# Performance work log

Measured on AMD Instinct MI355X. Metric: run time of the kernel, lower is better.

The kernel has to match this reference:

```python
import jax, jax.numpy as jnp
import numpy as np

PI = 3.1415927410125732
N = 4096
VELOCITY = 5e-7
RC = 3.15e-6          # collision radius
RR = 8e-6             # repulsion radius
RO = 2.5e-5           # orientation radius (Ra = inf -> inside_Ra all-true)
ALPHA = PI            # field of view; < 2*pi so within_view masking is active
DT_TRANS = 1.4e-14    # translational diffusion DT
DR = 0.0028
GAMMA = 25.0
DT = 0.2              # timestep dt
COLLISION_ITERS = 3   # fixed-iteration version of recursive solve_collisions
EPS = 1e-14


def _c(x):  # [N,2] real -> complex64
    return jax.lax.complex(x[..., 0], x[..., 1])


def _r(z):  # complex -> [..., 2] real
    return jnp.stack([z.real, z.imag], axis=-1)


def _anglediff(a, b):
    # torch get_anglediff: wrap angle(a)-angle(b) into (-pi, pi)
    diff = jnp.angle(a) - jnp.angle(b)
    diff = jnp.where(diff <= -PI, jnp.mod(diff, PI), diff)
    return diff - (diff >= PI) * (2.0 * PI)


def _cossim(a, b):
    # nn.CosineSimilarity(dim=1, eps=1e-14) on view_as_real of complex vectors
    dot = a.real * b.real + a.imag * b.imag
    na = jnp.sqrt(a.real ** 2 + a.imag ** 2 + 1e-30)
    nb = jnp.sqrt(b.real ** 2 + b.imag ** 2 + 1e-30)
    return dot / (jnp.maximum(na, EPS) * jnp.maximum(nb, EPS))


def setup_inputs() -> dict:
    key = jax.random.key(0)
    k1, k2, k3, k4, k5 = jax.random.split(key, 5)
    positions = jax.random.normal(k1, (N, 2), jnp.float32) * 5e-4
    ang = jax.random.uniform(k2, (N,), jnp.float32, -PI, PI)
    orientations = jnp.stack([jnp.cos(ang), jnp.sin(ang)], axis=-1)  # unit complex
    Deltas = jax.random.uniform(k3, (1,), jnp.float32, 0.1, 0.6)
    rot_noise = jax.random.normal(k4, (N,), jnp.float32)
    trans_noise = jax.random.normal(k5, (N, 2), jnp.float32)
    return {"positions": positions, "orientations": orientations, "Deltas": Deltas,
            "rot_noise": rot_noise, "trans_noise": trans_noise}


def reference(positions, orientations, Deltas, rot_noise, trans_noise):
    p = _c(positions)      # [N] complex positions
    u = _c(orientations)   # [N] complex orientations
    n = p.shape[0]
    eye = jnp.eye(n, dtype=bool)

    # pairwise direction/distance: dirs[i,j] = p_j - p_i
    dirs = p[None, :] - p[:, None]
    dists = jnp.abs(dirs)

    inside_Rr = (dists <= RR) & ~eye
    inside_Ro = dists <= RO + RC
    # inside_Ra with Ra = inf is all-True

    # angle between separation vector and orientation of the *neighbor* j
    ang_diff = _anglediff(dirs, u[None, :])
    in_front = ang_diff < PI / 2
    within_view = ang_diff < ALPHA  # alpha < 2*pi branch active

    cdtype = p.dtype
    mask_rr = (inside_Rr & in_front).astype(cdtype)
    mask_ra = within_view.astype(cdtype)  # inside_Ra all True
    mask_ro = (inside_Ro & within_view).astype(cdtype)

    n_r = mask_rr.real.sum(axis=1)
    S = (mask_rr @ p) / jnp.maximum(n_r, 1.0) - p * jnp.sign(n_r)
    d = -S

    n_a = mask_ra.real.sum(axis=1)
    cms = (mask_ra @ p) / jnp.maximum(n_a, 1.0)
    Ps = cms - p * jnp.sign(n_a)

    orientation_sums = mask_ro @ u

    leftturns = Ps * jnp.exp(1j * Deltas)
    rightturns = Ps * jnp.exp(-1j * Deltas)

    # T >= T_release branch: pick the turn most aligned with neighbor orientations
    left_closer = _cossim(leftturns, orientation_sums) >= _cossim(rightturns, orientation_sums)
    best_turns = jnp.where(left_closer, leftturns, rightturns)

    d_abs = jnp.abs(d)
    d_safe = jnp.where(d_abs > 0, d, jnp.ones((), cdtype))
    best_safe = jnp.where(jnp.abs(best_turns) > 0, best_turns, jnp.ones((), cdtype))
    angle_to_target = jnp.where(d_abs > 0, _anglediff(d_safe, u), _anglediff(best_safe, u))

    # rotational_noise = randn * sqrt(2*DR); rotation = exp(i*(dt*Gamma*DR*sin + noise*sqrt(dt)))
    rot = jnp.exp(1j * (DT * GAMMA * DR * jnp.sin(angle_to_target)
                        + rot_noise * np.float32(np.sqrt(2 * DR)) * np.float32(np.sqrt(DT))))

    # complex-normal translational noise (per-component std 1/sqrt(2)) * sqrt(2*DT) * sqrt(dt)
    tn = _c(trans_noise) * np.float32(np.sqrt(0.5)) * np.float32(np.sqrt(2 * DT_TRANS))
    translation = DT * VELOCITY * u + tn * np.float32(np.sqrt(DT))

    def collide(i, pos):
        dd = pos[None, :] - pos[:, None]
        dd_nd = jnp.where(eye, jnp.ones((), pos.dtype), dd)  # avoid 0/0 on diagonal
        ab = jnp.where(eye, 0.0, jnp.abs(dd_nd))
        coll = ab <= 2 * RC - jnp.eye(n, dtype=ab.dtype)
        safe = jnp.where(coll, ab, 1.0)
        move = jnp.where(coll, dd / safe * ((2.1 * RC - ab) * 0.5), jnp.zeros((), pos.dtype))
        return pos - move.sum(axis=1)

    new_p = jax.lax.fori_loop(0, COLLISION_ITERS, collide, p + translation)
    new_u = u * rot

    # pack the 5 complex outputs as real [5, N, 2]
    return jnp.stack([_r(new_p), _r(new_u), _r(orientation_sums), _r(leftturns), _r(rightturns)], axis=0)
```

## Files before the change

kernel.cpp:

```cpp
#include <hip/hip_runtime.h>
#include <math.h>

#define NPART 4096
#define NBLK  512
#define NTHR  256
#define IPB   8
#define SMAX  256
#define PPT   (NPART / NTHR)

constexpr float RORC   = (float)(2.5e-5 + 3.15e-6);
constexpr float RORC2  = RORC * RORC;
constexpr float RRF    = 8e-6f;
constexpr float RR2    = RRF * RRF;
constexpr float TWORC  = (float)(2.0 * 3.15e-6);
constexpr float TWORC2 = TWORC * TWORC;
constexpr float C21RC  = (float)(2.1 * 3.15e-6);
constexpr float RCAND2 = 1.6e-9f;
constexpr float C_ROT  = (float)(0.2 * 25.0 * 0.0028);
constexpr float C_RN1  = (float)0.07483314773547883;
constexpr float C_SQDT = (float)0.4472135954999579;
constexpr float C_TRV  = (float)(0.2 * 5e-7);
constexpr float C_HALF = (float)0.7071067811865476;
constexpr float C_SQ2T = (float)1.6733200530681511e-07;
constexpr float EPSF   = 1e-14f;

__global__ __launch_bounds__(NTHR, 2) void fused_all(
        const float2* __restrict__ pos, const float2* __restrict__ ori,
        const float* __restrict__ Deltas, const float* __restrict__ rot_noise,
        const float2* __restrict__ trans_noise, float2* __restrict__ out) {
    __shared__ float4   posL4[NPART / 2];
    __shared__ float4   oriL4[NPART / 2];
    __shared__ float    sred[2 * NTHR];
    __shared__ float    res[5][IPB];
    __shared__ unsigned bmap[NPART / 32];
    __shared__ int      Sidx[SMAX];
    __shared__ float4   posS4[SMAX / 2];
    __shared__ int      scnt;
    float2* posL = (float2*)posL4;
    float2* oriL = (float2*)oriL4;
    float2* posS = (float2*)posS4;

    const int tid  = threadIdx.x;
    const int il   = tid >> 6;
    const int lane = tid & 63;
    const int ia   = blockIdx.x * IPB + il;
    const int ib   = ia + 4;

    if (tid == 0) scnt = IPB;
    if (tid < IPB) Sidx[tid] = blockIdx.x * IPB + tid;
    if (tid < NPART / 32) bmap[tid] = 0u;

    float mx = 0.f, my = 0.f;
    #pragma unroll
    for (int k = 0; k < PPT; ++k) {
        const float2 v = pos[k * NTHR + tid];
        const float2 u = ori[k * NTHR + tid];
        posL[k * NTHR + tid] = v;
        oriL[k * NTHR + tid] = u;
        mx += v.x; my += v.y;
    }
    sred[tid] = mx; sred[NTHR + tid] = my;
    __syncthreads();

    const float2 pa = posL[ia];
    const float2 pb = posL[ib];
    float nrA = 0.f, sxA = 0.f, syA = 0.f, oxA = 0.f, oyA = 0.f;
    float nrB = 0.f, sxB = 0.f, syB = 0.f, oxB = 0.f, oyB = 0.f;
    #pragma unroll 2
    for (int t = lane; t < NPART / 2; t += 64) {
        const float4 w = posL4[t];
        const float dxa0 = w.x - pa.x, dya0 = w.y - pa.y;
        const float dxb0 = w.x - pb.x, dyb0 = w.y - pb.y;
        const float dxa1 = w.z - pa.x, dya1 = w.w - pa.y;
        const float dxb1 = w.z - pb.x, dyb1 = w.w - pb.y;
        const float r2a0 = fmaf(dxa0, dxa0, dya0 * dya0);
        const float r2b0 = fmaf(dxb0, dxb0, dyb0 * dyb0);
        const float r2a1 = fmaf(dxa1, dxa1, dya1 * dya1);
        const float r2b1 = fmaf(dxb1, dxb1, dyb1 * dyb1);

        if (r2a0 <= RCAND2 || r2b0 <= RCAND2) {
            const int j = 2 * t;
            atomicOr(&bmap[j >> 5], 1u << (j & 31));
        }
        if (r2a0 <= RORC2 || r2b0 <= RORC2) {
            const float2 uj = oriL[2 * t];
            if (r2a0 <= RORC2) {
                oxA += uj.x; oyA += uj.y;
                if (r2a0 <= RR2 && r2a0 > 0.f) {
                    const float dt_ = fmaf(dxa0, uj.x, dya0 * uj.y);
                    const float cr_ = fmaf(dya0, uj.x, -dxa0 * uj.y);
                    if (!((dt_ <= 0.f) && (cr_ >= 0.f))) {
                        nrA += 1.f; sxA += w.x; syA += w.y;
                    }
                }
            }
            if (r2b0 <= RORC2) {
                oxB += uj.x; oyB += uj.y;
                if (r2b0 <= RR2 && r2b0 > 0.f) {
                    const float dt_ = fmaf(dxb0, uj.x, dyb0 * uj.y);
                    const float cr_ = fmaf(dyb0, uj.x, -dxb0 * uj.y);
                    if (!((dt_ <= 0.f) && (cr_ >= 0.f))) {
                        nrB += 1.f; sxB += w.x; syB += w.y;
                    }
                }
            }
        }
        if (r2a1 <= RCAND2 || r2b1 <= RCAND2) {
            const int j = 2 * t + 1;
            atomicOr(&bmap[j >> 5], 1u << (j & 31));
        }
        if (r2a1 <= RORC2 || r2b1 <= RORC2) {
            const float2 uj = oriL[2 * t + 1];
            if (r2a1 <= RORC2) {
                oxA += uj.x; oyA += uj.y;
                if (r2a1 <= RR2 && r2a1 > 0.f) {
                    const float dt_ = fmaf(dxa1, uj.x, dya1 * uj.y);
                    const float cr_ = fmaf(dya1, uj.x, -dxa1 * uj.y);
                    if (!((dt_ <= 0.f) && (cr_ >= 0.f))) {
                        nrA += 1.f; sxA += w.z; syA += w.w;
                    }
                }
            }
            if (r2b1 <= RORC2) {
                oxB += uj.x; oyB += uj.y;
                if (r2b1 <= RR2 && r2b1 > 0.f) {
                    const float dt_ = fmaf(dxb1, uj.x, dyb1 * uj.y);
                    const float cr_ = fmaf(dyb1, uj.x, -dxb1 * uj.y);
                    if (!((dt_ <= 0.f) && (cr_ >= 0.f))) {
                        nrB += 1.f; sxB += w.z; syB += w.w;
                    }
                }
            }
        }
    }
    {
        float vals[10] = {nrA, sxA, syA, oxA, oyA, nrB, sxB, syB, oxB, oyB};
        #pragma unroll
        for (int q = 0; q < 10; ++q)
            #pragma unroll
            for (int off = 32; off >= 1; off >>= 1)
                vals[q] += __shfl_down(vals[q], off);
        if (lane == 0) {
            res[0][il]     = vals[0]; res[1][il]     = vals[1];
            res[2][il]     = vals[2]; res[3][il]     = vals[3];
            res[4][il]     = vals[4];
            res[0][il + 4] = vals[5]; res[1][il + 4] = vals[6];
            res[2][il + 4] = vals[7]; res[3][il + 4] = vals[8];
            res[4][il + 4] = vals[9];
        }
    }
    __syncthreads();

    if (tid < NPART / 32) {
        unsigned bits = bmap[tid];
        if (tid == (int)(blockIdx.x >> 2))
            bits &= ~(0xFFu << ((blockIdx.x & 3) * 8));
        while (bits) {
            const int b = __ffs(bits) - 1;
            bits &= bits - 1;
            const int slot = atomicAdd(&scnt, 1);
            if (slot < SMAX) Sidx[slot] = tid * 32 + b;
        }
    }
    __syncthreads();
    const int nS = (scnt < SMAX) ? scnt : SMAX;

    if (tid < nS) {
        const int p = Sidx[tid];
        const float2 pq = posL[p];
        const float2 uu = oriL[p];
        const float2 tn = trans_noise[p];
        posS[tid] = make_float2(
            pq.x + (C_TRV * uu.x + ((tn.x * C_HALF) * C_SQ2T) * C_SQDT),
            pq.y + (C_TRV * uu.y + ((tn.y * C_HALF) * C_SQ2T) * C_SQDT));
    }

    for (int s = NTHR / 2; s > 0; s >>= 1) {
        if (tid < s) { sred[tid] += sred[tid + s]; sred[NTHR + tid] += sred[NTHR + tid + s]; }
        __syncthreads();
    }
    const float cmx = sred[0]    * (1.f / NPART);
    const float cmy = sred[NTHR] * (1.f / NPART);

    if (tid < IPB) {
        const int g2 = blockIdx.x * IPB + tid;
        const float2 p = posL[g2];
        const float2 u = oriL[g2];
        const float nrv = res[0][tid], sxv = res[1][tid], syv = res[2][tid];
        const float osx = res[3][tid], osy = res[4][tid];

        const float inv = 1.f / fmaxf(nrv, 1.f);
        const float sg  = (nrv > 0.f) ? 1.f : 0.f;
        const float Sx = sxv * inv - p.x * sg;
        const float Sy = syv * inv - p.y * sg;
        const float dxv = -Sx, dyv = -Sy;

        const float Psx = cmx - p.x;
        const float Psy = cmy - p.y;

        float sd, cd;
        sincosf(Deltas[0], &sd, &cd);
        const float Lx = Psx * cd - Psy * sd;
        const float Ly = Psx * sd + Psy * cd;
        const float Rx = Psx * cd + Psy * sd;
        const float Ry = Psy * cd - Psx * sd;

        const float no  = fmaxf(sqrtf(osx * osx + osy * osy + 1e-30f), EPSF);
        const float nl  = fmaxf(sqrtf(Lx * Lx + Ly * Ly + 1e-30f), EPSF);
        const float nrr = fmaxf(sqrtf(Rx * Rx + Ry * Ry + 1e-30f), EPSF);
        const float csl = (Lx * osx + Ly * osy) / (nl * no);
        const float csr = (Rx * osx + Ry * osy) / (nrr * no);
        const bool left = (csl >= csr);
        const float bx = left ? Lx : Rx;
        const float by = left ? Ly : Ry;

        float cx, cy;
        if (dxv != 0.f || dyv != 0.f)    { cx = dxv; cy = dyv; }
        else if (bx != 0.f || by != 0.f) { cx = bx;  cy = by;  }
        else                             { cx = 1.f; cy = 0.f; }

        const float dt_ = cx * u.x + cy * u.y;
        const float cr_ = cy * u.x - cx * u.y;
        const float sin_t = cr_ / sqrtf(dt_ * dt_ + cr_ * cr_);

        const float ang = C_ROT * sin_t + (rot_noise[g2] * C_RN1) * C_SQDT;
        float sa, ca;
        sincosf(ang, &sa, &ca);
        out[1 * NPART + g2] = make_float2(u.x * ca - u.y * sa,
                                          u.x * sa + u.y * ca);
        out[2 * NPART + g2] = make_float2(osx, osy);
        out[3 * NPART + g2] = make_float2(Lx, Ly);
        out[4 * NPART + g2] = make_float2(Rx, Ry);
    }
    __syncthreads();

    for (int pass = 0; pass < 3; ++pass) {
        float px = 0.f, py = 0.f, ax = 0.f, ay = 0.f;
        const bool mv = (tid < nS);
        if (mv) { px = posS[tid].x; py = posS[tid].y; }
        int b = 0;
        for (; b + 4 <= nS; b += 4) {
            const float4 w0 = posS4[(b >> 1)];
            const float4 w1 = posS4[(b >> 1) + 1];
            const float bxs[4] = {w0.x, w0.z, w1.x, w1.z};
            const float bys[4] = {w0.y, w0.w, w1.y, w1.w};
            #pragma unroll
            for (int s = 0; s < 4; ++s) {
                if (mv) {
                    const float dx = bxs[s] - px, dy = bys[s] - py;
                    const float r2 = fmaf(dx, dx, dy * dy);
                    if (r2 <= TWORC2 && r2 > 0.f) {
                        const float ab = sqrtf(r2);
                        const float sc = (C21RC - ab) * 0.5f / ab;
                        ax = fmaf(dx, sc, ax);
                        ay = fmaf(dy, sc, ay);
                    }
                }
            }
        }
        for (; b < nS; ++b) {
            const float2 pb2 = posS[b];
            if (mv) {
                const float dx = pb2.x - px, dy = pb2.y - py;
                const float r2 = fmaf(dx, dx, dy * dy);
                if (r2 <= TWORC2 && r2 > 0.f) {
                    const float ab = sqrtf(r2);
                    const float sc = (C21RC - ab) * 0.5f / ab;
                    ax = fmaf(dx, sc, ax);
                    ay = fmaf(dy, sc, ay);
                }
            }
        }
        __syncthreads();
        if (mv) posS[tid] = make_float2(px - ax, py - ay);
        __syncthreads();
    }
    if (tid < IPB)
        out[0 * NPART + blockIdx.x * IPB + tid] = posS[tid];
}

extern "C" void kernel_launch(void* const* d_in, const int* in_sizes, int n_in,
                              void* d_out, int out_size, void* d_ws, size_t ws_size,
                              hipStream_t stream) {
    const float2* pos = (const float2*)d_in[0];
    const float2* ori = (const float2*)d_in[1];
    const float*  del = (const float*)d_in[2];
    const float*  rn  = (const float*)d_in[3];
    const float2* tn  = (const float2*)d_in[4];
    float2* o2 = (float2*)d_out;
    (void)d_ws; (void)ws_size;

    fused_all<<<dim3(NBLK), dim3(NTHR), 0, stream>>>(pos, ori, del, rn, tn, o2);
}
```

Measured before the change: 92.10 us.

## Stream pair positions from global memory instead of staging into LDS

Removes the 64KB LDS staging of positions and orientations, so the pair loop reads positions from global/L2 with explicit register double-buffering and fetches orientations on demand. The cut in LDS use lets launch_bounds rise to 4 blocks per CU for more occupancy. The center-of-mass reduction moves after the pair loop, becomes a partial tree plus a wavefront shuffle with fewer barriers, and one barrier before the collision passes is dropped. Scattered global reads of ori and more L2 traffic per block are the tradeoff.

```diff
diff --git a/kernel.cpp b/kernel.cpp
--- a/kernel.cpp
+++ b/kernel.cpp
@@ -24,21 +24,18 @@
 constexpr float C_SQ2T = (float)1.6733200530681511e-07;
 constexpr float EPSF   = 1e-14f;
 
-__global__ __launch_bounds__(NTHR, 2) void fused_all(
+__global__ __launch_bounds__(NTHR, 4) void fused_all(
         const float2* __restrict__ pos, const float2* __restrict__ ori,
         const float* __restrict__ Deltas, const float* __restrict__ rot_noise,
         const float2* __restrict__ trans_noise, float2* __restrict__ out) {
-    __shared__ float4   posL4[NPART / 2];
-    __shared__ float4   oriL4[NPART / 2];
     __shared__ float    sred[2 * NTHR];
     __shared__ float    res[5][IPB];
     __shared__ unsigned bmap[NPART / 32];
     __shared__ int      Sidx[SMAX];
     __shared__ float4   posS4[SMAX / 2];
     __shared__ int      scnt;
-    float2* posL = (float2*)posL4;
-    float2* oriL = (float2*)oriL4;
     float2* posS = (float2*)posS4;
+    const float4* __restrict__ pos4 = (const float4*)pos;
 
     const int tid  = threadIdx.x;
     const int il   = tid >> 6;
@@ -46,29 +43,20 @@
     const int ia   = blockIdx.x * IPB + il;
     const int ib   = ia + 4;
 
+    const float2 pa   = pos[ia];
+    const float2 pb   = pos[ib];
+    const float  delv = Deltas[0];
+    float rn_early = 0.f;
+    if (tid < IPB) rn_early = rot_noise[blockIdx.x * IPB + tid];
+
     if (tid == 0) scnt = IPB;
     if (tid < IPB) Sidx[tid] = blockIdx.x * IPB + tid;
     if (tid < NPART / 32) bmap[tid] = 0u;
-
-    float mx = 0.f, my = 0.f;
-    #pragma unroll
-    for (int k = 0; k < PPT; ++k) {
-        const float2 v = pos[k * NTHR + tid];
-        const float2 u = ori[k * NTHR + tid];
-        posL[k * NTHR + tid] = v;
-        oriL[k * NTHR + tid] = u;
-        mx += v.x; my += v.y;
-    }
-    sred[tid] = mx; sred[NTHR + tid] = my;
     __syncthreads();
 
-    const float2 pa = posL[ia];
-    const float2 pb = posL[ib];
     float nrA = 0.f, sxA = 0.f, syA = 0.f, oxA = 0.f, oyA = 0.f;
     float nrB = 0.f, sxB = 0.f, syB = 0.f, oxB = 0.f, oyB = 0.f;
-    #pragma unroll 2
-    for (int t = lane; t < NPART / 2; t += 64) {
-        const float4 w = posL4[t];
+    auto pair2 = [&](const float4& w, int jbase) {
         const float dxa0 = w.x - pa.x, dya0 = w.y - pa.y;
         const float dxb0 = w.x - pb.x, dyb0 = w.y - pb.y;
         const float dxa1 = w.z - pa.x, dya1 = w.w - pa.y;
@@ -79,11 +67,10 @@
         const float r2b1 = fmaf(dxb1, dxb1, dyb1 * dyb1);
 
         if (r2a0 <= RCAND2 || r2b0 <= RCAND2) {
-            const int j = 2 * t;
-            atomicOr(&bmap[j >> 5], 1u << (j & 31));
+            atomicOr(&bmap[jbase >> 5], 1u << (jbase & 31));
         }
         if (r2a0 <= RORC2 || r2b0 <= RORC2) {
-            const float2 uj = oriL[2 * t];
+            const float2 uj = ori[jbase];
             if (r2a0 <= RORC2) {
                 oxA += uj.x; oyA += uj.y;
                 if (r2a0 <= RR2 && r2a0 > 0.f) {
@@ -106,11 +93,11 @@
             }
         }
         if (r2a1 <= RCAND2 || r2b1 <= RCAND2) {
-            const int j = 2 * t + 1;
-            atomicOr(&bmap[j >> 5], 1u << (j & 31));
+            const int j1 = jbase + 1;
+            atomicOr(&bmap[j1 >> 5], 1u << (j1 & 31));
         }
         if (r2a1 <= RORC2 || r2b1 <= RORC2) {
-            const float2 uj = oriL[2 * t + 1];
+            const float2 uj = ori[jbase + 1];
             if (r2a1 <= RORC2) {
                 oxA += uj.x; oyA += uj.y;
                 if (r2a1 <= RR2 && r2a1 > 0.f) {
@@ -131,6 +118,24 @@
                     }
                 }
             }
+        }
+    };
+    {
+        float4 wb0 = pos4[lane],       wb1 = pos4[lane + 64];
+        float4 wb2 = pos4[lane + 128], wb3 = pos4[lane + 192];
+        #pragma unroll
+        for (int bi = 0; bi < 8; ++bi) {
+            const int t0 = lane + bi * 256;
+            float4 wn0, wn1, wn2, wn3;
+            if (bi < 7) {
+                wn0 = pos4[t0 + 256]; wn1 = pos4[t0 + 320];
+                wn2 = pos4[t0 + 384]; wn3 = pos4[t0 + 448];
+            }
+            pair2(wb0, 2 * t0);
+            pair2(wb1, 2 * (t0 + 64));
+            pair2(wb2, 2 * (t0 + 128));
+            pair2(wb3, 2 * (t0 + 192));
+            if (bi < 7) { wb0 = wn0; wb1 = wn1; wb2 = wn2; wb3 = wn3; }
         }
     }
     {
@@ -149,9 +154,19 @@
             res[4][il + 4] = vals[9];
         }
     }
+
+    float mx = 0.f, my = 0.f;
+    #pragma unroll
+    for (int k = 0; k < PPT; ++k) {
+        const float2 v = pos[k * NTHR + tid];
+        mx += v.x; my += v.y;
+    }
+    sred[tid] = mx; sred[NTHR + tid] = my;
     __syncthreads();
 
-    if (tid < NPART / 32) {
+    if (tid < 128) {
+        sred[tid]        += sred[tid + 128];
+        sred[NTHR + tid] += sred[NTHR + tid + 128];
         unsigned bits = bmap[tid];
         if (tid == (int)(blockIdx.x >> 2))
             bits &= ~(0xFFu << ((blockIdx.x & 3) * 8));
@@ -165,27 +180,38 @@
     __syncthreads();
     const int nS = (scnt < SMAX) ? scnt : SMAX;
 
+    if (tid < 64) {
+        sred[tid]        += sred[tid + 64];
+        sred[NTHR + tid] += sred[NTHR + tid + 64];
+    }
     if (tid < nS) {
         const int p = Sidx[tid];
-        const float2 pq = posL[p];
-        const float2 uu = oriL[p];
+        const float2 pq = pos[p];
+        const float2 uu = ori[p];
         const float2 tn = trans_noise[p];
         posS[tid] = make_float2(
             pq.x + (C_TRV * uu.x + ((tn.x * C_HALF) * C_SQ2T) * C_SQDT),
             pq.y + (C_TRV * uu.y + ((tn.y * C_HALF) * C_SQ2T) * C_SQDT));
     }
-
-    for (int s = NTHR / 2; s > 0; s >>= 1) {
-        if (tid < s) { sred[tid] += sred[tid + s]; sred[NTHR + tid] += sred[NTHR + tid + s]; }
-        __syncthreads();
-    }
-    const float cmx = sred[0]    * (1.f / NPART);
-    const float cmy = sred[NTHR] * (1.f / NPART);
+    __syncthreads();
+
+    float cmx = 0.f, cmy = 0.f;
+    if (il == 0) {
+        float vx = sred[lane];
+        float vy = sred[NTHR + lane];
+        #pragma unroll
+        for (int off = 32; off >= 1; off >>= 1) {
+            vx += __shfl_down(vx, off);
+            vy += __shfl_down(vy, off);
+        }
+        cmx = __shfl(vx, 0) * (1.f / NPART);
+        cmy = __shfl(vy, 0) * (1.f / NPART);
+    }
 
     if (tid < IPB) {
         const int g2 = blockIdx.x * IPB + tid;
-        const float2 p = posL[g2];
-        const float2 u = oriL[g2];
+        const float2 p = pos[g2];
+        const float2 u = ori[g2];
         const float nrv = res[0][tid], sxv = res[1][tid], syv = res[2][tid];
         const float osx = res[3][tid], osy = res[4][tid];
 
@@ -199,7 +225,7 @@
         const float Psy = cmy - p.y;
 
         float sd, cd;
-        sincosf(Deltas[0], &sd, &cd);
+        sincosf(delv, &sd, &cd);
         const float Lx = Psx * cd - Psy * sd;
         const float Ly = Psx * sd + Psy * cd;
         const float Rx = Psx * cd + Psy * sd;
@@ -223,7 +249,7 @@
         const float cr_ = cy * u.x - cx * u.y;
         const float sin_t = cr_ / sqrtf(dt_ * dt_ + cr_ * cr_);
 
-        const float ang = C_ROT * sin_t + (rot_noise[g2] * C_RN1) * C_SQDT;
+        const float ang = C_ROT * sin_t + (rn_early * C_RN1) * C_SQDT;
         float sa, ca;
         sincosf(ang, &sa, &ca);
         out[1 * NPART + g2] = make_float2(u.x * ca - u.y * sa,
@@ -232,30 +258,33 @@
         out[3 * NPART + g2] = make_float2(Lx, Ly);
         out[4 * NPART + g2] = make_float2(Rx, Ry);
     }
-    __syncthreads();
 
     for (int pass = 0; pass < 3; ++pass) {
         float px = 0.f, py = 0.f, ax = 0.f, ay = 0.f;
         const bool mv = (tid < nS);
         if (mv) { px = posS[tid].x; py = posS[tid].y; }
         int b = 0;
-        for (; b + 4 <= nS; b += 4) {
-            const float4 w0 = posS4[(b >> 1)];
-            const float4 w1 = posS4[(b >> 1) + 1];
-            const float bxs[4] = {w0.x, w0.z, w1.x, w1.z};
-            const float bys[4] = {w0.y, w0.w, w1.y, w1.w};
-            #pragma unroll
-            for (int s = 0; s < 4; ++s) {
-                if (mv) {
-                    const float dx = bxs[s] - px, dy = bys[s] - py;
-                    const float r2 = fmaf(dx, dx, dy * dy);
-                    if (r2 <= TWORC2 && r2 > 0.f) {
-                        const float ab = sqrtf(r2);
-                        const float sc = (C21RC - ab) * 0.5f / ab;
-                        ax = fmaf(dx, sc, ax);
-                        ay = fmaf(dy, sc, ay);
-                    }
-                }
+        if (b + 4 <= nS) {
+            float4 c0 = posS4[0], c1 = posS4[1];
+            for (; b + 4 <= nS; b += 4) {
+                float4 n0, n1;
+                if (b + 8 <= nS) { n0 = posS4[(b >> 1) + 2]; n1 = posS4[(b >> 1) + 3]; }
+                const float bxs[4] = {c0.x, c0.z, c1.x, c1.z};
+                const float bys[4] = {c0.y, c0.w, c1.y, c1.w};
+                #pragma unroll
+                for (int s = 0; s < 4; ++s) {
+                    if (mv) {
+                        const float dx = bxs[s] - px, dy = bys[s] - py;
+                        const float r2 = fmaf(dx, dx, dy * dy);
+                        if (r2 <= TWORC2 && r2 > 0.f) {
+                            const float ab = sqrtf(r2);
+                            const float sc = (C21RC - ab) * 0.5f / ab;
+                            ax = fmaf(dx, sc, ax);
+                            ay = fmaf(dy, sc, ay);
+                        }
+                    }
+                }
+                if (b + 8 <= nS) { c0 = n0; c1 = n1; }
             }
         }
         for (; b < nS; ++b) {
```

After: 90.34 us. No clear change (-1.9%).
